# Performance work log

Hardware: AMD Instinct MI355X
Metric: run time of the kernel (lower is better)

Reference implementation:

```python
import jax, jax.numpy as jnp
import numpy as np

B, T, D, H = 4, 2048, 1024, 16
DH = D // H  # head dim = 64

def setup_inputs() -> dict:
    key = jax.random.key(0)
    k1, k2, k3, k4, k5, k6 = jax.random.split(key, 6)
    x = jax.random.normal(k1, (B, T, D), dtype=jnp.float32)
    mask = jax.random.randint(k2, (B, 1, 1, T), 0, 2, dtype=jnp.int32)
    # nn.Linear(out_dim, out_dim*3): weight stored here as [in, out]
    W_qkv = jax.random.normal(k3, (D, 3 * D), dtype=jnp.float32) * (1.0 / np.sqrt(D))
    b_qkv = jax.random.normal(k4, (3 * D,), dtype=jnp.float32) * 0.02
    W_out = jax.random.normal(k5, (D, D), dtype=jnp.float32) * (1.0 / np.sqrt(D))
    b_out = jax.random.normal(k6, (D,), dtype=jnp.float32) * 0.02
    return {"x": x, "mask": mask, "W_qkv": W_qkv, "b_qkv": b_qkv,
            "W_out": W_out, "b_out": b_out}

def reference(x, mask, W_qkv, b_qkv, W_out, b_out):
    # QKV projection: [B,T,3D]
    qkv = x @ W_qkv + b_qkv
    q, k, v = qkv[..., :D], qkv[..., D:2 * D], qkv[..., 2 * D:]
    # split heads -> [B,H,T,DH]
    def split(t):
        return t.reshape(B, T, H, DH).transpose(0, 2, 1, 3)
    q, k, v = split(q), split(k), split(v)
    # scaled dot-product attention (scale = sqrt(head_dim), per torch source)
    scores = jnp.einsum('bhqd,bhkd->bhqk', q, k) / jnp.sqrt(jnp.float32(DH))
    scores = jnp.where(mask == 0, jnp.float32(-1000.0), scores)
    weights = jax.nn.softmax(scores, axis=-1)  # dropout = identity (eval mode)
    out = jnp.einsum('bhqk,bhkd->bhqd', weights, v)
    out = out.transpose(0, 2, 1, 3).reshape(B, T, D)
    return out @ W_out + b_out
```

## Files before the change

### kernel.cpp

```cpp
#include <hip/hip_runtime.h>
#include <hip/hip_bf16.h>
#include <stdint.h>

#define B_  4
#define T_  2048
#define D_  1024
#define H_  16
#define DH_ 64

typedef _Float16 half8 __attribute__((ext_vector_type(8)));
typedef _Float16 half4 __attribute__((ext_vector_type(4)));
typedef __fp16   fp16x2 __attribute__((ext_vector_type(2)));
typedef float    f32x4 __attribute__((ext_vector_type(4)));

#define MFMA16(a, b, c) __builtin_amdgcn_mfma_f32_16x16x32_f16(a, b, c, 0, 0, 0)

__device__ static inline void gload_lds16(const void* g, void* l) {
  __builtin_amdgcn_global_load_lds(
      (const __attribute__((address_space(1))) void*)g,
      (__attribute__((address_space(3))) void*)l, 16, 0, 0);
}

__global__ void convert_f32_f16(const float* __restrict__ in, _Float16* __restrict__ out, long n) {
  long i = ((long)blockIdx.x * blockDim.x + threadIdx.x) * 4;
  long stride = (long)gridDim.x * blockDim.x * 4;
  for (; i < n; i += stride) {
    float4 v = *(const float4*)(in + i);
    half4 hv;
    hv.x = (_Float16)v.x; hv.y = (_Float16)v.y; hv.z = (_Float16)v.z; hv.w = (_Float16)v.w;
    *(half4*)(out + i) = hv;
  }
}

__global__ void make_maskh(const int* __restrict__ mask, _Float16* __restrict__ mh, int n) {
  int i = blockIdx.x * blockDim.x + threadIdx.x;
  if (i < n) mh[i] = mask[i] ? (_Float16)1.0f : (_Float16)0.0f;
}

__global__ void transpose_f32_f16(const float* __restrict__ in, _Float16* __restrict__ out,
                                  int K, int N) {
  __shared__ float tile[32][33];
  int n0 = blockIdx.x * 32, k0 = blockIdx.y * 32;
  int x = threadIdx.x, y = threadIdx.y;
  #pragma unroll
  for (int j = 0; j < 32; j += 8)
    tile[y + j][x] = in[(long)(k0 + y + j) * N + n0 + x];
  __syncthreads();
  #pragma unroll
  for (int j = 0; j < 32; j += 8)
    out[(long)(n0 + y + j) * K + k0 + x] = (_Float16)tile[x][y + j];
}

template <int EPI>
__global__ __launch_bounds__(256, 2)
void mha_gemm2(const _Float16* __restrict__ A, const _Float16* __restrict__ Bt,
               const float* __restrict__ bias, const _Float16* __restrict__ mhp,
               _Float16* __restrict__ qo, _Float16* __restrict__ ko, _Float16* __restrict__ vo,
               float* __restrict__ co, int M, int N, int K, int gx) {
  __shared__ _Float16 shbuf[16384];
  _Float16* const As = shbuf;
  _Float16* const Bs = shbuf + 8192;
  const int t = threadIdx.x;
  const int l = t & 63;
  const int w = t >> 6;
  const int wr = w >> 1, wc = w & 1;

  const int cpx = gridDim.x >> 3;
  const int wg = (blockIdx.x & 7) * cpx + (blockIdx.x >> 3);
  const int m0 = (wg / gx) * 128, n0 = (wg % gx) * 128;

  const _Float16* ag[4];
  const _Float16* bg[4];
  #pragma unroll
  for (int j = 0; j < 4; ++j) {
    int c = j * 256 + t;
    int row = c >> 3, sub = c & 7;
    int s = (sub ^ (row & 7)) * 8;
    ag[j] = A  + (long)(m0 + row) * K + s;
    bg[j] = Bt + (long)(n0 + row) * K + s;
  }

  f32x4 acc[4][4];
  #pragma unroll
  for (int f = 0; f < 4; ++f)
    #pragma unroll
    for (int g = 0; g < 4; ++g) acc[f][g] = (f32x4){0.f, 0.f, 0.f, 0.f};

  const int hi = l >> 4;

  for (int k0 = 0; k0 < K; k0 += 64) {
    #pragma unroll
    for (int j = 0; j < 4; ++j) {
      gload_lds16(ag[j] + k0, &As[j * 2048 + w * 512]);
      gload_lds16(bg[j] + k0, &Bs[j * 2048 + w * 512]);
    }
    __syncthreads();
    half8 af[2][4], bf[2][4];
    #pragma unroll
    for (int kk = 0; kk < 2; ++kk)
      #pragma unroll
      for (int f = 0; f < 4; ++f) {
        int ra = wr * 64 + f * 16 + (l & 15);
        int rb = wc * 64 + f * 16 + (l & 15);
        af[kk][f] = *(const half8*)((const char*)As + ra * 128 +
                                    ((((kk << 2) | hi) ^ (ra & 7)) << 4));
        bf[kk][f] = *(const half8*)((const char*)Bs + rb * 128 +
                                    ((((kk << 2) | hi) ^ (rb & 7)) << 4));
      }
    #pragma unroll
    for (int kk = 0; kk < 2; ++kk)
      #pragma unroll
      for (int f = 0; f < 4; ++f)
        #pragma unroll
        for (int g = 0; g < 4; ++g)
          acc[f][g] = MFMA16(af[kk][f], bf[kk][g], acc[f][g]);
    __syncthreads();
  }

  if constexpr (EPI == 0) {
    if (n0 >= 2 * D_) {
      const int bb = m0 >> 11, m0t = m0 & 2047;
      #pragma unroll
      for (int g = 0; g < 4; ++g) {
        int colL = wc * 64 + g * 16 + (l & 15);
        float bv = bias[n0 + colL];
        int swz = (colL & 7) << 4;
        #pragma unroll
        for (int f = 0; f < 4; ++f) {
          int row0 = wr * 64 + f * 16 + hi * 4;
          half4 hv;
          #pragma unroll
          for (int r = 0; r < 4; ++r) {
            float mv = (float)mhp[bb * T_ + m0t + row0 + r];
            hv[r] = (_Float16)((acc[f][g][r] + bv) * mv);
          }
          *(half4*)&shbuf[colL * 128 + (row0 ^ swz)] = hv;
        }
      }
      __syncthreads();
      #pragma unroll
      for (int i = 0; i < 8; ++i) {
        int e = i * 256 + t;
        int colL = e >> 4, chunk = e & 15;
        int swz = (colL & 7) << 4;
        half8 v8 = *(const half8*)&shbuf[colL * 128 + ((chunk * 8) ^ swz)];
        int d = (n0 + colL) & 1023;
        int h2 = d >> 6, dh = d & 63;
        *(half8*)&vo[(((long)bb * H_ + h2) * DH_ + dh) * T_ + m0t + chunk * 8] = v8;
      }
    } else {
      #pragma unroll
      for (int g = 0; g < 4; ++g) {
        int j = n0 + wc * 64 + g * 16 + (l & 15);
        float bv = bias[j];
        int which = j >> 10;
        int d = j & 1023;
        int h = d >> 6, dh = d & 63;
        _Float16* base = which == 0 ? qo : ko;
        float sc = which == 0 ? 0.1803368801f : 1.0f;
        #pragma unroll
        for (int f = 0; f < 4; ++f) {
          int row0 = m0 + wr * 64 + f * 16 + ((l >> 4) << 2);
          #pragma unroll
          for (int r = 0; r < 4; ++r) {
            int row = row0 + r;
            int bb = row >> 11, tt = row & 2047;
            base[(((long)bb * H_ + h) * T_ + tt) * DH_ + dh] =
                (_Float16)((acc[f][g][r] + bv) * sc);
          }
        }
      }
    }
  } else {
    #pragma unroll
    for (int g = 0; g < 4; ++g) {
      int j = n0 + wc * 64 + g * 16 + (l & 15);
      float bv = bias[j];
      #pragma unroll
      for (int f = 0; f < 4; ++f) {
        int row0 = m0 + wr * 64 + f * 16 + ((l >> 4) << 2);
        #pragma unroll
        for (int r = 0; r < 4; ++r)
          co[(long)(row0 + r) * N + j] = acc[f][g][r] + bv;
      }
    }
  }
}

__global__ __launch_bounds__(128, 2)
void mha_attn7(const _Float16* __restrict__ Q, const _Float16* __restrict__ K,
               const _Float16* __restrict__ Vt, const _Float16* __restrict__ mh,
               _Float16* __restrict__ out) {
  __shared__ _Float16 Ksh[2][4096];
  __shared__ _Float16 Vsh[2][4096];
  const int t = threadIdx.x, l = t & 63, w = t >> 6;
  const int hi = l >> 4, q = l & 15;

  const int bid = blockIdx.x;
  const int idx = bid >> 3;
  const int bh = (bid & 7) * 8 + (idx >> 4);
  const int qt = idx & 15;
  const int b = bh >> 4, h = bh & 15;
  const long base = (long)bh * (T_ * DH_);
  const int qb = qt * 128 + w * 64;

  half8 qf[4][2];
  #pragma unroll
  for (int G = 0; G < 4; ++G) {
    qf[G][0] = *(const half8*)(Q + base + (long)(qb + G * 16 + q) * DH_ + hi * 8);
    qf[G][1] = *(const half8*)(Q + base + (long)(qb + G * 16 + q) * DH_ + hi * 8 + 32);
  }

  const _Float16* ks[4];
  const _Float16* vs[4];
  #pragma unroll
  for (int j = 0; j < 4; ++j) {
    int c = w * 256 + j * 64 + l;
    int row = c >> 3, sub = c & 7;
    int s = (sub ^ ((row & 7) ^ ((row >> 2) & 7))) * 8;
    ks[j] = K  + base + row * DH_ + s;
    vs[j] = Vt + base + (long)row * T_ + s;
  }

  int kcb[4];
  #pragma unroll
  for (int g = 0; g < 4; ++g) {
    int kr = (g >> 1) * 32 + (q >> 2) * 8 + (g & 1) * 4 + (q & 3);
    int sw = (kr & 7) ^ ((kr >> 2) & 7);
    kcb[g] = kr * 128 + ((hi * 16) ^ (sw << 4));
  }
  int vcb[4];
  #pragma unroll
  for (int o = 0; o < 4; ++o) {
    int vr = o * 16 + q;
    int sw = (vr & 7) ^ ((vr >> 2) & 7);
    vcb[o] = vr * 128 + ((hi * 16) ^ (sw << 4));
  }

  const _Float16* mrow = mh + b * T_ + hi * 8;

  f32x4 acc[4][4], accD[4];
  #pragma unroll
  for (int G = 0; G < 4; ++G) {
    accD[G] = (f32x4){0.f, 0.f, 0.f, 0.f};
    #pragma unroll
    for (int o = 0; o < 4; ++o) acc[G][o] = (f32x4){0.f, 0.f, 0.f, 0.f};
  }

#define STAGEKV(BI, TT) do {                                                 \
    _Pragma("unroll")                                                        \
    for (int j = 0; j < 4; ++j) {                                            \
      gload_lds16(ks[j] + (TT) * (64 * DH_), &Ksh[BI][w * 2048 + j * 512]);  \
      gload_lds16(vs[j] + (TT) * 64,         &Vsh[BI][w * 2048 + j * 512]);  \
    }                                                                        \
  } while (0)

  STAGEKV(0, 0);
  __syncthreads();

  for (int kt = 0; kt < T_ / 64; ++kt) {
    const int bi = kt & 1;
    if (kt + 1 < T_ / 64) STAGEKV(bi ^ 1, kt + 1);

    const half8 mf0 = *(const half8*)(mrow + kt * 64);
    const half8 mf1 = *(const half8*)(mrow + kt * 64 + 32);

    const char* kbb = (const char*)Ksh[bi];
    const char* vbb = (const char*)Vsh[bi];
    half8 kf[4][2];
    #pragma unroll
    for (int g = 0; g < 4; ++g) {
      kf[g][0] = *(const half8*)(kbb + kcb[g]);
      kf[g][1] = *(const half8*)(kbb + (kcb[g] ^ 64));
    }
    half8 vf[4][2];
    #pragma unroll
    for (int o = 0; o < 4; ++o) {
      vf[o][0] = *(const half8*)(vbb + vcb[o]);
      vf[o][1] = *(const half8*)(vbb + (vcb[o] ^ 64));
    }

    #pragma unroll
    for (int G = 0; G < 4; ++G) {
      __builtin_amdgcn_s_setprio(1);
      f32x4 z[4];
      #pragma unroll
      for (int g = 0; g < 4; ++g) {
        f32x4 zz = (f32x4){0.f, 0.f, 0.f, 0.f};
        zz = MFMA16(kf[g][0], qf[G][0], zz);
        z[g] = MFMA16(kf[g][1], qf[G][1], zz);
      }
      __builtin_amdgcn_s_setprio(0);
      union { fp16x2 h2[4]; half8 h8; } u0, u1;
      #pragma unroll
      for (int i = 0; i < 2; ++i) {
        u0.h2[i]     = __builtin_amdgcn_cvt_pkrtz(__builtin_amdgcn_exp2f(z[0][2*i]),
                                                  __builtin_amdgcn_exp2f(z[0][2*i+1]));
        u0.h2[2 + i] = __builtin_amdgcn_cvt_pkrtz(__builtin_amdgcn_exp2f(z[1][2*i]),
                                                  __builtin_amdgcn_exp2f(z[1][2*i+1]));
        u1.h2[i]     = __builtin_amdgcn_cvt_pkrtz(__builtin_amdgcn_exp2f(z[2][2*i]),
                                                  __builtin_amdgcn_exp2f(z[2][2*i+1]));
        u1.h2[2 + i] = __builtin_amdgcn_cvt_pkrtz(__builtin_amdgcn_exp2f(z[3][2*i]),
                                                  __builtin_amdgcn_exp2f(z[3][2*i+1]));
      }
      __builtin_amdgcn_s_setprio(1);
      accD[G] = MFMA16(u0.h8, mf0, accD[G]);
      accD[G] = MFMA16(u1.h8, mf1, accD[G]);
      #pragma unroll
      for (int o = 0; o < 4; ++o) {
        acc[G][o] = MFMA16(u0.h8, vf[o][0], acc[G][o]);
        acc[G][o] = MFMA16(u1.h8, vf[o][1], acc[G][o]);
      }
      __builtin_amdgcn_s_setprio(0);
    }
    __syncthreads();
  }
#undef STAGEKV

  #pragma unroll
  for (int G = 0; G < 4; ++G)
    #pragma unroll
    for (int r = 0; r < 4; ++r) {
      float inv = __builtin_amdgcn_rcpf(accD[G][r]);
      int trow = qb + G * 16 + hi * 4 + r;
      #pragma unroll
      for (int o = 0; o < 4; ++o)
        out[((long)b * T_ + trow) * D_ + h * DH_ + o * 16 + q] =
            (_Float16)(acc[G][o][r] * inv);
    }
}

extern "C" void kernel_launch(void* const* d_in, const int* in_sizes, int n_in,
                              void* d_out, int out_size, void* d_ws, size_t ws_size,
                              hipStream_t stream) {
  const float* x    = (const float*)d_in[0];
  const int*   mask = (const int*)d_in[1];
  const float* wqkv = (const float*)d_in[2];
  const float* bqkv = (const float*)d_in[3];
  const float* wout = (const float*)d_in[4];
  const float* bout = (const float*)d_in[5];
  float* out = (float*)d_out;

  _Float16* ws = (_Float16*)d_ws;
  const long nX = (long)B_ * T_ * D_;
  _Float16* xh    = ws;
  _Float16* wqkvt = xh + nX;
  _Float16* woutt = wqkvt + (long)D_ * 3 * D_;
  _Float16* mh    = woutt + (long)D_ * D_;
  _Float16* Qb    = woutt + (long)D_ * D_ + 16384;
  _Float16* Kb    = Qb + nX;
  _Float16* Vtg   = Kb + nX;
  _Float16* attnh = Vtg + nX;

  convert_f32_f16<<<2048, 256, 0, stream>>>(x, xh, nX);
  make_maskh<<<(B_ * T_) / 256, 256, 0, stream>>>(mask, mh, B_ * T_);
  transpose_f32_f16<<<dim3(3 * D_ / 32, D_ / 32), dim3(32, 8), 0, stream>>>(wqkv, wqkvt, D_, 3 * D_);
  transpose_f32_f16<<<dim3(D_ / 32, D_ / 32), dim3(32, 8), 0, stream>>>(wout, woutt, D_, D_);

  mha_gemm2<0><<<1536, 256, 0, stream>>>(
      xh, wqkvt, bqkv, mh, Qb, Kb, Vtg, nullptr, B_ * T_, 3 * D_, D_, 24);

  mha_attn7<<<1024, 128, 0, stream>>>(Qb, Kb, Vtg, mh, attnh);

  mha_gemm2<1><<<512, 256, 0, stream>>>(
      attnh, woutt, bout, nullptr, nullptr, nullptr, nullptr, out, B_ * T_, D_, D_, 8);
}
```

Baseline: 179.1 us.

## Replace QKV GEMM with 256x256-tile 8-wave double-buffered pipelined kernel

The QKV projection GEMM moves to a new kernel with 256x256 output tiles, 512 threads and 128KB of shared memory. It double-buffers K-tiles loaded directly into LDS and splits each K-step into four phases that interleave the next tile's loads with MFMA work, raising wave priority during MFMA. The larger tiles raise arithmetic intensity and the pipelining is meant to hide global-load latency. In exchange, occupancy drops to one block per CU and the grid shrinks to 384 blocks, which may leave some CUs underused. The output GEMM is split into its own non-templated kernel with unchanged logic.

```diff
diff --git a/kernel.cpp b/kernel.cpp
--- a/kernel.cpp
+++ b/kernel.cpp
@@ -51,15 +51,163 @@
     out[(long)(n0 + y + j) * K + k0 + x] = (_Float16)tile[x][y + j];
 }
 
-template <int EPI>
+__global__ __launch_bounds__(512)
+void mha_gemm8(const _Float16* __restrict__ A, const _Float16* __restrict__ Bt,
+               const float* __restrict__ bias, const _Float16* __restrict__ mhp,
+               _Float16* __restrict__ qo, _Float16* __restrict__ ko,
+               _Float16* __restrict__ vo) {
+  __shared__ _Float16 shbuf[65536];
+  const int tid = threadIdx.x;
+  const int l = tid & 63, w = tid >> 6;
+  const int wm = w >> 2, wn = w & 3;
+  const int hi = l >> 4, q = l & 15;
+  const int K = D_;
+
+  const int cpx = gridDim.x >> 3;
+  const int wg = (blockIdx.x & 7) * cpx + (blockIdx.x >> 3);
+  const int m0 = (wg / 12) * 256, n0 = (wg % 12) * 256;
+  const int bb = m0 >> 11, m0t = m0 & 2047;
+
+  const int srow = tid >> 3, ssub = tid & 7;
+  const int ssw = ssub ^ (srow & 7);
+  const _Float16* a0 = A  + (long)(m0 + srow) * K + ssw * 8;
+  const _Float16* b0 = Bt + (long)(n0 + srow) * K + ssw * 8;
+  _Float16* lA = shbuf + tid * 8;
+  _Float16* lB = shbuf + 32768 + tid * 8;
+  const long joff = (long)64 * K;
+
+#define STG_A(S, T) do { _Pragma("unroll")                                   \
+    for (int j = 0; j < 4; ++j)                                              \
+      gload_lds16(a0 + (T) * 64 + j * joff, lA + (S) * 16384 + j * 4096);    \
+  } while (0)
+#define STG_B(S, T) do { _Pragma("unroll")                                   \
+    for (int j = 0; j < 4; ++j)                                              \
+      gload_lds16(b0 + (T) * 64 + j * joff, lB + (S) * 16384 + j * 4096);    \
+  } while (0)
+
+  f32x4 acc[8][4];
+  #pragma unroll
+  for (int f = 0; f < 8; ++f)
+    #pragma unroll
+    for (int g = 0; g < 4; ++g) acc[f][g] = (f32x4){0.f, 0.f, 0.f, 0.f};
+
+  const char* const Abase = (const char*)shbuf;
+  const char* const Bbase = (const char*)shbuf + 65536;
+
+  STG_A(0, 0); STG_B(0, 0);
+  asm volatile("s_waitcnt vmcnt(0)" ::: "memory");
+  asm volatile("s_barrier" ::: "memory");
+
+  half8 bf[2][4];
+
+#define PHASE(S, QD, STG_STMT, DO_WAIT) do {                                 \
+    if ((QD) == 0) {                                                         \
+      _Pragma("unroll")                                                      \
+      for (int g = 0; g < 4; ++g) {                                          \
+        int rb = wn * 64 + g * 16 + q;                                       \
+        _Pragma("unroll")                                                    \
+        for (int kk = 0; kk < 2; ++kk)                                       \
+          bf[kk][g] = *(const half8*)(Bbase + (S) * 32768 + rb * 128 +       \
+                                      ((((kk << 2) | hi) ^ (rb & 7)) << 4)); \
+      }                                                                      \
+    }                                                                        \
+    half8 af[2][2];                                                          \
+    _Pragma("unroll")                                                        \
+    for (int f2 = 0; f2 < 2; ++f2) {                                         \
+      int ra = wm * 128 + ((QD) * 2 + f2) * 16 + q;                          \
+      _Pragma("unroll")                                                      \
+      for (int kk = 0; kk < 2; ++kk)                                         \
+        af[kk][f2] = *(const half8*)(Abase + (S) * 32768 + ra * 128 +        \
+                                     ((((kk << 2) | hi) ^ (ra & 7)) << 4));  \
+    }                                                                        \
+    STG_STMT;                                                                \
+    asm volatile("s_barrier" ::: "memory");                                  \
+    __builtin_amdgcn_s_setprio(1);                                           \
+    _Pragma("unroll")                                                        \
+    for (int kk = 0; kk < 2; ++kk)                                           \
+      _Pragma("unroll")                                                      \
+      for (int f2 = 0; f2 < 2; ++f2)                                         \
+        _Pragma("unroll")                                                    \
+        for (int g = 0; g < 4; ++g)                                          \
+          acc[(QD) * 2 + f2][g] =                                            \
+              MFMA16(af[kk][f2], bf[kk][g], acc[(QD) * 2 + f2][g]);          \
+    __builtin_amdgcn_s_setprio(0);                                           \
+    if (DO_WAIT) asm volatile("s_waitcnt vmcnt(0)" ::: "memory");            \
+    asm volatile("s_barrier" ::: "memory");                                  \
+  } while (0)
+
+  for (int i = 0; i < 8; ++i) {
+    const int t1 = 2 * i + 1, t2 = 2 * i + 2;
+    PHASE(0, 0, STG_A(1, t1), 0);
+    PHASE(0, 1, STG_B(1, t1), 0);
+    PHASE(0, 2, (void)0, 0);
+    PHASE(0, 3, (void)0, 1);
+    PHASE(1, 0, if (i < 7) STG_A(0, t2), 0);
+    PHASE(1, 1, if (i < 7) STG_B(0, t2), 0);
+    PHASE(1, 2, (void)0, 0);
+    PHASE(1, 3, (void)0, 1);
+  }
+#undef PHASE
+#undef STG_A
+#undef STG_B
+
+  if (n0 >= 2 * D_) {
+    #pragma unroll
+    for (int g = 0; g < 4; ++g) {
+      int colL = wn * 64 + g * 16 + q;
+      float bv = bias[n0 + colL];
+      int swz = (colL & 7) << 3;
+      #pragma unroll
+      for (int fr = 0; fr < 8; ++fr) {
+        int rowL = wm * 128 + fr * 16 + hi * 4;
+        half4 hv;
+        #pragma unroll
+        for (int r = 0; r < 4; ++r) {
+          float mv = (float)mhp[bb * T_ + m0t + rowL + r];
+          hv[r] = (_Float16)((acc[fr][g][r] + bv) * mv);
+        }
+        *(half4*)&shbuf[colL * 256 + (rowL ^ swz)] = hv;
+      }
+    }
+    __syncthreads();
+    #pragma unroll
+    for (int it = 0; it < 16; ++it) {
+      int e = it * 512 + tid;
+      int colL = e >> 5, chunk = e & 31;
+      int swz = (colL & 7) << 3;
+      half8 v8 = *(const half8*)&shbuf[colL * 256 + ((chunk * 8) ^ swz)];
+      int d = (n0 + colL) & 1023;
+      int h2 = d >> 6, dh = d & 63;
+      *(half8*)&vo[(((long)bb * H_ + h2) * DH_ + dh) * T_ + m0t + chunk * 8] = v8;
+    }
+  } else {
+    #pragma unroll
+    for (int g = 0; g < 4; ++g) {
+      int j = n0 + wn * 64 + g * 16 + q;
+      float bv = bias[j];
+      int which = j >> 10;
+      int d = j & 1023;
+      int h = d >> 6, dh = d & 63;
+      _Float16* base = which == 0 ? qo : ko;
+      float sc = which == 0 ? 0.1803368801f : 1.0f;
+      #pragma unroll
+      for (int fr = 0; fr < 8; ++fr) {
+        int rowL = m0t + wm * 128 + fr * 16 + hi * 4;
+        #pragma unroll
+        for (int r = 0; r < 4; ++r)
+          base[(((long)bb * H_ + h) * T_ + rowL + r) * DH_ + dh] =
+              (_Float16)((acc[fr][g][r] + bv) * sc);
+      }
+    }
+  }
+}
+
 __global__ __launch_bounds__(256, 2)
-void mha_gemm2(const _Float16* __restrict__ A, const _Float16* __restrict__ Bt,
-               const float* __restrict__ bias, const _Float16* __restrict__ mhp,
-               _Float16* __restrict__ qo, _Float16* __restrict__ ko, _Float16* __restrict__ vo,
-               float* __restrict__ co, int M, int N, int K, int gx) {
-  __shared__ _Float16 shbuf[16384];
-  _Float16* const As = shbuf;
-  _Float16* const Bs = shbuf + 8192;
+void mha_gemm_out(const _Float16* __restrict__ A, const _Float16* __restrict__ Bt,
+                  const float* __restrict__ bias, float* __restrict__ co,
+                  int M, int N, int K, int gx) {
+  __shared__ _Float16 As[128 * 64];
+  __shared__ _Float16 Bs[128 * 64];
   const int t = threadIdx.x;
   const int l = t & 63;
   const int w = t >> 6;
@@ -117,72 +265,16 @@
     __syncthreads();
   }
 
-  if constexpr (EPI == 0) {
-    if (n0 >= 2 * D_) {
-      const int bb = m0 >> 11, m0t = m0 & 2047;
-      #pragma unroll
-      for (int g = 0; g < 4; ++g) {
-        int colL = wc * 64 + g * 16 + (l & 15);
-        float bv = bias[n0 + colL];
-        int swz = (colL & 7) << 4;
-        #pragma unroll
-        for (int f = 0; f < 4; ++f) {
-          int row0 = wr * 64 + f * 16 + hi * 4;
-          half4 hv;
-          #pragma unroll
-          for (int r = 0; r < 4; ++r) {
-            float mv = (float)mhp[bb * T_ + m0t + row0 + r];
-            hv[r] = (_Float16)((acc[f][g][r] + bv) * mv);
-          }
-          *(half4*)&shbuf[colL * 128 + (row0 ^ swz)] = hv;
-        }
-      }
-      __syncthreads();
-      #pragma unroll
-      for (int i = 0; i < 8; ++i) {
-        int e = i * 256 + t;
-        int colL = e >> 4, chunk = e & 15;
-        int swz = (colL & 7) << 4;
-        half8 v8 = *(const half8*)&shbuf[colL * 128 + ((chunk * 8) ^ swz)];
-        int d = (n0 + colL) & 1023;
-        int h2 = d >> 6, dh = d & 63;
-        *(half8*)&vo[(((long)bb * H_ + h2) * DH_ + dh) * T_ + m0t + chunk * 8] = v8;
-      }
-    } else {
-      #pragma unroll
-      for (int g = 0; g < 4; ++g) {
-        int j = n0 + wc * 64 + g * 16 + (l & 15);
-        float bv = bias[j];
-        int which = j >> 10;
-        int d = j & 1023;
-        int h = d >> 6, dh = d & 63;
-        _Float16* base = which == 0 ? qo : ko;
-        float sc = which == 0 ? 0.1803368801f : 1.0f;
-        #pragma unroll
-        for (int f = 0; f < 4; ++f) {
-          int row0 = m0 + wr * 64 + f * 16 + ((l >> 4) << 2);
-          #pragma unroll
-          for (int r = 0; r < 4; ++r) {
-            int row = row0 + r;
-            int bb = row >> 11, tt = row & 2047;
-            base[(((long)bb * H_ + h) * T_ + tt) * DH_ + dh] =
-                (_Float16)((acc[f][g][r] + bv) * sc);
-          }
-        }
-      }
-    }
-  } else {
-    #pragma unroll
-    for (int g = 0; g < 4; ++g) {
-      int j = n0 + wc * 64 + g * 16 + (l & 15);
-      float bv = bias[j];
-      #pragma unroll
-      for (int f = 0; f < 4; ++f) {
-        int row0 = m0 + wr * 64 + f * 16 + ((l >> 4) << 2);
-        #pragma unroll
-        for (int r = 0; r < 4; ++r)
-          co[(long)(row0 + r) * N + j] = acc[f][g][r] + bv;
-      }
+  #pragma unroll
+  for (int g = 0; g < 4; ++g) {
+    int j = n0 + wc * 64 + g * 16 + (l & 15);
+    float bv = bias[j];
+    #pragma unroll
+    for (int f = 0; f < 4; ++f) {
+      int row0 = m0 + wr * 64 + f * 16 + ((l >> 4) << 2);
+      #pragma unroll
+      for (int r = 0; r < 4; ++r)
+        co[(long)(row0 + r) * N + j] = acc[f][g][r] + bv;
     }
   }
 }
@@ -357,11 +449,9 @@
   transpose_f32_f16<<<dim3(3 * D_ / 32, D_ / 32), dim3(32, 8), 0, stream>>>(wqkv, wqkvt, D_, 3 * D_);
   transpose_f32_f16<<<dim3(D_ / 32, D_ / 32), dim3(32, 8), 0, stream>>>(wout, woutt, D_, D_);
 
-  mha_gemm2<0><<<1536, 256, 0, stream>>>(
-      xh, wqkvt, bqkv, mh, Qb, Kb, Vtg, nullptr, B_ * T_, 3 * D_, D_, 24);
+  mha_gemm8<<<384, 512, 0, stream>>>(xh, wqkvt, bqkv, mh, Qb, Kb, Vtg);
 
   mha_attn7<<<1024, 128, 0, stream>>>(Qb, Kb, Vtg, mh, attnh);
 
-  mha_gemm2<1><<<512, 256, 0, stream>>>(
-      attnh, woutt, bout, nullptr, nullptr, nullptr, nullptr, out, B_ * T_, D_, D_, 8);
-}
+  mha_gemm_out<<<512, 256, 0, stream>>>(attnh, woutt, bout, out, B_ * T_, D_, D_, 8);
+}
```

Result: no change. 180.4 us (+0.7%).
